# Performance work log

Hardware: AMD Instinct MI355X
Metric: run time of the kernel (lower is better)

Reference implementation:

```python
import jax, jax.numpy as jnp
import numpy as np

EMBED_DIMS = 1024
NUM_HEADS = 16
HEAD_DIMS = EMBED_DIMS // NUM_HEADS


def setup_inputs() -> dict:
    key = jax.random.key(0)
    k_x, k_wqkv, k_bqkv, k_wp, k_bp = jax.random.split(key, 5)
    B, N, D = 2, 2048, EMBED_DIMS
    x = jax.random.normal(k_x, (B, N, D), dtype=jnp.float32)
    # torch nn.Linear(in, out): weight [out, in], y = x @ W.T + b
    s = 1.0 / np.sqrt(D)
    W_qkv = jax.random.uniform(k_wqkv, (3 * D, D), jnp.float32, -s, s)
    b_qkv = jax.random.uniform(k_bqkv, (3 * D,), jnp.float32, -s, s)
    W_proj = jax.random.uniform(k_wp, (D, D), jnp.float32, -s, s)
    b_proj = jax.random.uniform(k_bp, (D,), jnp.float32, -s, s)
    return {"x": x, "W_qkv": W_qkv, "b_qkv": b_qkv, "W_proj": W_proj, "b_proj": b_proj}


def reference(x, W_qkv, b_qkv, W_proj, b_proj):
    B, N, D = x.shape
    H, Hd = NUM_HEADS, HEAD_DIMS
    # qkv projection: [B, N, 3, H, Hd] -> split q, k, v as [B, H, N, Hd]
    qkv = (x @ W_qkv.T + b_qkv).reshape(B, N, 3, H, Hd).transpose(2, 0, 3, 1, 4)
    q, k, v = qkv[0], qkv[1], qkv[2]
    scale = 1.0 / jnp.sqrt(jnp.asarray(Hd, x.dtype))
    attn = jnp.einsum("bhqd,bhkd->bhqk", q, k) * scale  # [B, H, N, N]
    attn = jax.nn.softmax(attn, axis=-1)
    out = jnp.einsum("bhqk,bhkd->bhqd", attn, v)  # [B, H, N, Hd]
    out = out.transpose(0, 2, 1, 3).reshape(B, N, D)
    out = out @ W_proj.T + b_proj
    return out
```

## Files before the change

### kernel.cpp

```cpp
#include <hip/hip_runtime.h>

typedef _Float16 f16x8 __attribute__((ext_vector_type(8)));
typedef __attribute__((ext_vector_type(4))) float f32x4;

static __device__ __forceinline__ unsigned short f2h(float f) {
  return __builtin_bit_cast(unsigned short, (_Float16)f);
}

#if __has_builtin(__builtin_amdgcn_exp2f)
#define EXP2(x) __builtin_amdgcn_exp2f(x)
#else
#define EXP2(x) exp2f(x)
#endif

#define GLOAD_LDS16(gp, lp)                                          \
  __builtin_amdgcn_global_load_lds(                                  \
      (const __attribute__((address_space(1))) unsigned int*)(gp),   \
      (__attribute__((address_space(3))) unsigned int*)(lp), 16, 0, 0)

__global__ __launch_bounds__(256) void cvt_all(
    const float* __restrict__ X, const float* __restrict__ Wq,
    const float* __restrict__ Wp, unsigned short* __restrict__ Xb,
    unsigned short* __restrict__ Wqb, unsigned short* __restrict__ Wpb) {
  const int i = blockIdx.x * 256 + threadIdx.x;
  const float4* src;
  unsigned short* dst;
  int off;
  if (i < 1048576) {
    src = (const float4*)X; dst = Xb; off = i;
  } else if (i < 1835008) {
    src = (const float4*)Wq; dst = Wqb; off = i - 1048576;
  } else {
    src = (const float4*)Wp; dst = Wpb; off = i - 1835008;
  }
  const float4 v = src[off];
  *(ushort4*)(dst + (size_t)off * 4) =
      make_ushort4(f2h(v.x), f2h(v.y), f2h(v.z), f2h(v.w));
}

__global__ __launch_bounds__(256) void qkv_gemm(
    const unsigned short* __restrict__ Xb, const unsigned short* __restrict__ Wb,
    const float* __restrict__ bias, unsigned short* __restrict__ Qb,
    unsigned short* __restrict__ Kb, unsigned short* __restrict__ Vt) {
  __shared__ __align__(16) unsigned short A_sh[128 * 32];
  __shared__ __align__(16) unsigned short B_sh[128 * 32];
  const int n0 = blockIdx.x * 128, m0 = blockIdx.y * 128;
  const int tid = threadIdx.x, lane = tid & 63, wave = tid >> 6;
  const int wr = wave >> 1, wc = wave & 1, lm = lane & 15, lg = lane >> 4;
  const int lrow = lane >> 2, lcol = (lane & 3) * 8;

  f32x4 acc[4][4] = {};

  for (int k0 = 0; k0 < 1024; k0 += 32) {
#pragma unroll
    for (int j = 0; j < 2; ++j) {
      const int chunk = wave * 2 + j;
      const int row = chunk * 16 + lrow;
      GLOAD_LDS16(Xb + (size_t)(m0 + row) * 1024 + k0 + lcol, &A_sh[chunk * 512]);
      GLOAD_LDS16(Wb + (size_t)(n0 + row) * 1024 + k0 + lcol, &B_sh[chunk * 512]);
    }
    __syncthreads();
    f16x8 af[4], bfr[4];
#pragma unroll
    for (int mi = 0; mi < 4; ++mi)
      af[mi] = *(const f16x8*)&A_sh[(wr * 64 + mi * 16 + lm) * 32 + lg * 8];
#pragma unroll
    for (int ni = 0; ni < 4; ++ni)
      bfr[ni] = *(const f16x8*)&B_sh[(wc * 64 + ni * 16 + lm) * 32 + lg * 8];
#pragma unroll
    for (int mi = 0; mi < 4; ++mi)
#pragma unroll
      for (int ni = 0; ni < 4; ++ni)
        acc[mi][ni] = __builtin_amdgcn_mfma_f32_16x16x32_f16(
            af[mi], bfr[ni], acc[mi][ni], 0, 0, 0);
    __syncthreads();
  }

  const float qscale = 0.18033688011112042f;
#pragma unroll
  for (int mi = 0; mi < 4; ++mi) {
#pragma unroll
    for (int ni = 0; ni < 4; ++ni) {
      const int gn = n0 + wc * 64 + ni * 16 + lm;
      const float bv = bias[gn];
      const int which = gn >> 10;
      const int h = (gn >> 6) & 15;
      const int hd = gn & 63;
      float v[4];
#pragma unroll
      for (int r = 0; r < 4; ++r) v[r] = acc[mi][ni][r] + bv;
      const int gm0 = m0 + wr * 64 + mi * 16 + lg * 4;
      const int bb = gm0 >> 11;
      const int nq0 = gm0 & 2047;
      if (which == 0) {
        unsigned short* p = Qb + (((size_t)bb * 16 + h) * 2048 + nq0) * 64 + hd;
        p[0] = f2h(v[0] * qscale);   p[64] = f2h(v[1] * qscale);
        p[128] = f2h(v[2] * qscale); p[192] = f2h(v[3] * qscale);
      } else if (which == 1) {
        unsigned short* p = Kb + (((size_t)bb * 16 + h) * 2048 + nq0) * 64 + hd;
        p[0] = f2h(v[0]);   p[64] = f2h(v[1]);
        p[128] = f2h(v[2]); p[192] = f2h(v[3]);
      } else {
        *(ushort4*)(Vt + (((size_t)bb * 16 + h) * 64 + hd) * 2048 + nq0) =
            make_ushort4(f2h(v[0]), f2h(v[1]), f2h(v[2]), f2h(v[3]));
      }
    }
  }
}

__global__ __launch_bounds__(256) void attn_kernel(
    const unsigned short* __restrict__ Qb, const unsigned short* __restrict__ Kb,
    const unsigned short* __restrict__ Vt, unsigned short* __restrict__ Ob) {
  __shared__ __align__(16) unsigned short K_sh[2][2][64 * 32];
  __shared__ __align__(16) unsigned short V_sh[2][2][64 * 32];
  __shared__ __align__(16) unsigned short P_sh[128 * 68];
  const int bh = blockIdx.y, q0 = blockIdx.x * 128;
  const size_t base = (size_t)bh * (2048 * 64);
  const unsigned short* Qp = Qb + base;
  const unsigned short* Kp = Kb + base;
  const unsigned short* Vp = Vt + base;
  const int tid = threadIdx.x, lane = tid & 63, wave = tid >> 6;
  const int lm = lane & 15, lg = lane >> 4;
  const int r4 = lane >> 2;
  const int sg8 = (((lane & 3) ^ ((r4 >> 1) & 3)) * 8);
  const int lgx = (lg ^ ((lm >> 1) & 3)) * 8;

  f16x8 qf[2][2];
#pragma unroll
  for (int mi = 0; mi < 2; ++mi)
#pragma unroll
    for (int kc = 0; kc < 2; ++kc)
      qf[mi][kc] = *(const f16x8*)(Qp +
          (size_t)(q0 + wave * 32 + mi * 16 + lm) * 64 + kc * 32 + lg * 8);

  f32x4 o[2][4] = {};
  float lsum[2][4] = {};

  const int plane = wave & 1;
  const bool isV = wave >= 2;

#define STAGE(kt_, b_)                                                        \
  do {                                                                        \
    if (!isV) {                                                               \
      _Pragma("unroll")                                                       \
      for (int qv = 0; qv < 4; ++qv)                                          \
        GLOAD_LDS16(Kp + (size_t)((kt_) * 64 + qv * 16 + r4) * 64 +           \
                        plane * 32 + sg8,                                     \
                    &K_sh[b_][plane][qv * 512]);                              \
    } else {                                                                  \
      _Pragma("unroll")                                                       \
      for (int qv = 0; qv < 4; ++qv)                                          \
        GLOAD_LDS16(Vp + (size_t)(qv * 16 + r4) * 2048 + (kt_) * 64 +         \
                        plane * 32 + sg8,                                     \
                    &V_sh[b_][plane][qv * 512]);                              \
    }                                                                         \
  } while (0)

  STAGE(0, 0);

  for (int kt = 0; kt < 32; ++kt) {
    const int cur = kt & 1;
    __syncthreads();
    if (kt < 31) STAGE(kt + 1, cur ^ 1);

    f32x4 s[2][4] = {};
#pragma unroll
    for (int kc = 0; kc < 2; ++kc) {
#pragma unroll
      for (int ni = 0; ni < 4; ++ni) {
        const f16x8 kf =
            *(const f16x8*)&K_sh[cur][kc][(ni * 16 + lm) * 32 + lgx];
#pragma unroll
        for (int mi = 0; mi < 2; ++mi)
          s[mi][ni] = __builtin_amdgcn_mfma_f32_16x16x32_f16(
              qf[mi][kc], kf, s[mi][ni], 0, 0, 0);
      }
    }

#pragma unroll
    for (int mi = 0; mi < 2; ++mi)
#pragma unroll
      for (int ni = 0; ni < 4; ++ni) {
        float p0 = EXP2(s[mi][ni][0]), p1 = EXP2(s[mi][ni][1]);
        float p2 = EXP2(s[mi][ni][2]), p3 = EXP2(s[mi][ni][3]);
        lsum[mi][0] += p0; lsum[mi][1] += p1;
        lsum[mi][2] += p2; lsum[mi][3] += p3;
        unsigned short* pp =
            &P_sh[(wave * 32 + mi * 16 + lg * 4) * 68 + ni * 16 + lm];
        pp[0] = f2h(p0);    pp[68] = f2h(p1);
        pp[136] = f2h(p2);  pp[204] = f2h(p3);
      }

#pragma unroll
    for (int kc = 0; kc < 2; ++kc) {
      f16x8 pa[2];
#pragma unroll
      for (int mi = 0; mi < 2; ++mi)
        pa[mi] = *(const f16x8*)&P_sh[(wave * 32 + mi * 16 + lm) * 68 +
                                      kc * 32 + lg * 8];
#pragma unroll
      for (int ni = 0; ni < 4; ++ni) {
        const f16x8 vb =
            *(const f16x8*)&V_sh[cur][kc][(ni * 16 + lm) * 32 + lgx];
#pragma unroll
        for (int mi = 0; mi < 2; ++mi)
          o[mi][ni] = __builtin_amdgcn_mfma_f32_16x16x32_f16(
              pa[mi], vb, o[mi][ni], 0, 0, 0);
      }
    }
  }
#undef STAGE

  const int b = bh >> 4, h = bh & 15;
#pragma unroll
  for (int mi = 0; mi < 2; ++mi)
#pragma unroll
    for (int r = 0; r < 4; ++r) {
      float l = lsum[mi][r];
      l += __shfl_xor(l, 1);
      l += __shfl_xor(l, 2);
      l += __shfl_xor(l, 4);
      l += __shfl_xor(l, 8);
      const float inv = 1.0f / l;
      const int nq = q0 + wave * 32 + mi * 16 + lg * 4 + r;
      unsigned short* p = Ob + ((size_t)(b * 2048 + nq) * 16 + h) * 64 + lm;
      p[0] = f2h(o[mi][0][r] * inv);
      p[16] = f2h(o[mi][1][r] * inv);
      p[32] = f2h(o[mi][2][r] * inv);
      p[48] = f2h(o[mi][3][r] * inv);
    }
}

__global__ __launch_bounds__(256) void proj_gemm(
    const unsigned short* __restrict__ A, const unsigned short* __restrict__ Wb,
    const float* __restrict__ bias, float* __restrict__ Out) {
  __shared__ __align__(16) unsigned short A_sh[64 * 32];
  __shared__ __align__(16) unsigned short B_sh[128 * 32];
  const int n0 = blockIdx.x * 128, m0 = blockIdx.y * 64;
  const int tid = threadIdx.x, lane = tid & 63, wave = tid >> 6;
  const int wr = wave >> 1, wc = wave & 1, lm = lane & 15, lg = lane >> 4;
  const int lrow = lane >> 2, lcol = (lane & 3) * 8;

  f32x4 acc[2][4] = {};

  for (int k0 = 0; k0 < 1024; k0 += 32) {
    {
      const int row = wave * 16 + lrow;
      GLOAD_LDS16(A + (size_t)(m0 + row) * 1024 + k0 + lcol, &A_sh[wave * 512]);
    }
#pragma unroll
    for (int j = 0; j < 2; ++j) {
      const int chunk = wave * 2 + j;
      const int row = chunk * 16 + lrow;
      GLOAD_LDS16(Wb + (size_t)(n0 + row) * 1024 + k0 + lcol, &B_sh[chunk * 512]);
    }
    __syncthreads();
    f16x8 af[2], bfr[4];
#pragma unroll
    for (int mi = 0; mi < 2; ++mi)
      af[mi] = *(const f16x8*)&A_sh[(wr * 32 + mi * 16 + lm) * 32 + lg * 8];
#pragma unroll
    for (int ni = 0; ni < 4; ++ni)
      bfr[ni] = *(const f16x8*)&B_sh[(wc * 64 + ni * 16 + lm) * 32 + lg * 8];
#pragma unroll
    for (int mi = 0; mi < 2; ++mi)
#pragma unroll
      for (int ni = 0; ni < 4; ++ni)
        acc[mi][ni] = __builtin_amdgcn_mfma_f32_16x16x32_f16(
            af[mi], bfr[ni], acc[mi][ni], 0, 0, 0);
    __syncthreads();
  }

#pragma unroll
  for (int mi = 0; mi < 2; ++mi)
#pragma unroll
    for (int ni = 0; ni < 4; ++ni) {
      const int gn = n0 + wc * 64 + ni * 16 + lm;
      const float bv = bias[gn];
#pragma unroll
      for (int r = 0; r < 4; ++r) {
        const int gm = m0 + wr * 32 + mi * 16 + lg * 4 + r;
        Out[(size_t)gm * 1024 + gn] = acc[mi][ni][r] + bv;
      }
    }
}

extern "C" void kernel_launch(void* const* d_in, const int* in_sizes, int n_in,
                              void* d_out, int out_size, void* d_ws, size_t ws_size,
                              hipStream_t stream) {
  const float* x      = (const float*)d_in[0];
  const float* W_qkv  = (const float*)d_in[1];
  const float* b_qkv  = (const float*)d_in[2];
  const float* W_proj = (const float*)d_in[3];
  const float* b_proj = (const float*)d_in[4];
  float* out = (float*)d_out;

  unsigned short* Qb  = (unsigned short*)d_ws;
  unsigned short* Kb  = Qb + 4194304;
  unsigned short* Vt  = Kb + 4194304;
  unsigned short* Ao  = Vt + 4194304;
  unsigned short* Xb  = Ao + 4194304;
  unsigned short* Wqb = Xb + 4194304;
  unsigned short* Wpb = Wqb + 3145728;

  cvt_all<<<8192, 256, 0, stream>>>(x, W_qkv, W_proj, Xb, Wqb, Wpb);
  qkv_gemm<<<dim3(24, 32), 256, 0, stream>>>(Xb, Wqb, b_qkv, Qb, Kb, Vt);
  attn_kernel<<<dim3(16, 32), 256, 0, stream>>>(Qb, Kb, Vt, Ao);
  proj_gemm<<<dim3(8, 64), 256, 0, stream>>>(Ao, Wpb, b_proj, out);
}
```

Before: 197.8 us.

## Widen GEMM K-step with swizzled LDS and halve attention query tile

The QKV and projection GEMMs now load a 64-wide K slab per iteration into two 32-wide LDS planes, using an XOR-swizzled layout. This halves the number of barrier pairs per K loop and aims to reduce LDS bank conflicts. The attention kernel drops from 128 to 64 query rows per block, with 16 rows per wave, which doubles the grid to improve occupancy and wave count across CUs. The cost is that each block now streams the full K/V sequence for fewer query rows, so K/V traffic per unit of work doubles, and the larger GEMM LDS footprint may lower occupancy.

```diff
diff --git a/kernel.cpp b/kernel.cpp
--- a/kernel.cpp
+++ b/kernel.cpp
@@ -42,37 +42,47 @@
     const unsigned short* __restrict__ Xb, const unsigned short* __restrict__ Wb,
     const float* __restrict__ bias, unsigned short* __restrict__ Qb,
     unsigned short* __restrict__ Kb, unsigned short* __restrict__ Vt) {
-  __shared__ __align__(16) unsigned short A_sh[128 * 32];
-  __shared__ __align__(16) unsigned short B_sh[128 * 32];
+  __shared__ __align__(16) unsigned short A_sh[2][128 * 32];
+  __shared__ __align__(16) unsigned short B_sh[2][128 * 32];
   const int n0 = blockIdx.x * 128, m0 = blockIdx.y * 128;
   const int tid = threadIdx.x, lane = tid & 63, wave = tid >> 6;
   const int wr = wave >> 1, wc = wave & 1, lm = lane & 15, lg = lane >> 4;
-  const int lrow = lane >> 2, lcol = (lane & 3) * 8;
+  const int r4 = lane >> 2;
+  const int sg8 = (((lane & 3) ^ ((r4 >> 1) & 3)) * 8);
+  const int lgx = (lg ^ ((lm >> 1) & 3)) * 8;
 
   f32x4 acc[4][4] = {};
 
-  for (int k0 = 0; k0 < 1024; k0 += 32) {
+  for (int k0 = 0; k0 < 1024; k0 += 64) {
 #pragma unroll
     for (int j = 0; j < 2; ++j) {
       const int chunk = wave * 2 + j;
-      const int row = chunk * 16 + lrow;
-      GLOAD_LDS16(Xb + (size_t)(m0 + row) * 1024 + k0 + lcol, &A_sh[chunk * 512]);
-      GLOAD_LDS16(Wb + (size_t)(n0 + row) * 1024 + k0 + lcol, &B_sh[chunk * 512]);
-    }
-    __syncthreads();
-    f16x8 af[4], bfr[4];
-#pragma unroll
-    for (int mi = 0; mi < 4; ++mi)
-      af[mi] = *(const f16x8*)&A_sh[(wr * 64 + mi * 16 + lm) * 32 + lg * 8];
-#pragma unroll
-    for (int ni = 0; ni < 4; ++ni)
-      bfr[ni] = *(const f16x8*)&B_sh[(wc * 64 + ni * 16 + lm) * 32 + lg * 8];
-#pragma unroll
-    for (int mi = 0; mi < 4; ++mi)
+      const int row = chunk * 16 + r4;
+#pragma unroll
+      for (int p = 0; p < 2; ++p) {
+        GLOAD_LDS16(Xb + (size_t)(m0 + row) * 1024 + k0 + p * 32 + sg8,
+                    &A_sh[p][chunk * 512]);
+        GLOAD_LDS16(Wb + (size_t)(n0 + row) * 1024 + k0 + p * 32 + sg8,
+                    &B_sh[p][chunk * 512]);
+      }
+    }
+    __syncthreads();
+#pragma unroll
+    for (int kc = 0; kc < 2; ++kc) {
+      f16x8 af[4], bfr[4];
+#pragma unroll
+      for (int mi = 0; mi < 4; ++mi)
+        af[mi] = *(const f16x8*)&A_sh[kc][(wr * 64 + mi * 16 + lm) * 32 + lgx];
 #pragma unroll
       for (int ni = 0; ni < 4; ++ni)
-        acc[mi][ni] = __builtin_amdgcn_mfma_f32_16x16x32_f16(
-            af[mi], bfr[ni], acc[mi][ni], 0, 0, 0);
+        bfr[ni] = *(const f16x8*)&B_sh[kc][(wc * 64 + ni * 16 + lm) * 32 + lgx];
+#pragma unroll
+      for (int mi = 0; mi < 4; ++mi)
+#pragma unroll
+        for (int ni = 0; ni < 4; ++ni)
+          acc[mi][ni] = __builtin_amdgcn_mfma_f32_16x16x32_f16(
+              af[mi], bfr[ni], acc[mi][ni], 0, 0, 0);
+    }
     __syncthreads();
   }
 
@@ -113,8 +123,8 @@
     const unsigned short* __restrict__ Vt, unsigned short* __restrict__ Ob) {
   __shared__ __align__(16) unsigned short K_sh[2][2][64 * 32];
   __shared__ __align__(16) unsigned short V_sh[2][2][64 * 32];
-  __shared__ __align__(16) unsigned short P_sh[128 * 68];
-  const int bh = blockIdx.y, q0 = blockIdx.x * 128;
+  __shared__ __align__(16) unsigned short P_sh[64 * 68];
+  const int bh = blockIdx.y, q0 = blockIdx.x * 64;
   const size_t base = (size_t)bh * (2048 * 64);
   const unsigned short* Qp = Qb + base;
   const unsigned short* Kp = Kb + base;
@@ -125,16 +135,14 @@
   const int sg8 = (((lane & 3) ^ ((r4 >> 1) & 3)) * 8);
   const int lgx = (lg ^ ((lm >> 1) & 3)) * 8;
 
-  f16x8 qf[2][2];
-#pragma unroll
-  for (int mi = 0; mi < 2; ++mi)
-#pragma unroll
-    for (int kc = 0; kc < 2; ++kc)
-      qf[mi][kc] = *(const f16x8*)(Qp +
-          (size_t)(q0 + wave * 32 + mi * 16 + lm) * 64 + kc * 32 + lg * 8);
-
-  f32x4 o[2][4] = {};
-  float lsum[2][4] = {};
+  f16x8 qf[2];
+#pragma unroll
+  for (int kc = 0; kc < 2; ++kc)
+    qf[kc] = *(const f16x8*)(Qp +
+        (size_t)(q0 + wave * 16 + lm) * 64 + kc * 32 + lg * 8);
+
+  f32x4 o[4] = {};
+  float lsum[4] = {};
 
   const int plane = wave & 1;
   const bool isV = wave >= 2;
@@ -163,49 +171,36 @@
     __syncthreads();
     if (kt < 31) STAGE(kt + 1, cur ^ 1);
 
-    f32x4 s[2][4] = {};
+    f32x4 s[4] = {};
 #pragma unroll
     for (int kc = 0; kc < 2; ++kc) {
 #pragma unroll
       for (int ni = 0; ni < 4; ++ni) {
         const f16x8 kf =
             *(const f16x8*)&K_sh[cur][kc][(ni * 16 + lm) * 32 + lgx];
-#pragma unroll
-        for (int mi = 0; mi < 2; ++mi)
-          s[mi][ni] = __builtin_amdgcn_mfma_f32_16x16x32_f16(
-              qf[mi][kc], kf, s[mi][ni], 0, 0, 0);
-      }
-    }
-
-#pragma unroll
-    for (int mi = 0; mi < 2; ++mi)
-#pragma unroll
-      for (int ni = 0; ni < 4; ++ni) {
-        float p0 = EXP2(s[mi][ni][0]), p1 = EXP2(s[mi][ni][1]);
-        float p2 = EXP2(s[mi][ni][2]), p3 = EXP2(s[mi][ni][3]);
-        lsum[mi][0] += p0; lsum[mi][1] += p1;
-        lsum[mi][2] += p2; lsum[mi][3] += p3;
-        unsigned short* pp =
-            &P_sh[(wave * 32 + mi * 16 + lg * 4) * 68 + ni * 16 + lm];
-        pp[0] = f2h(p0);    pp[68] = f2h(p1);
-        pp[136] = f2h(p2);  pp[204] = f2h(p3);
-      }
+        s[ni] = __builtin_amdgcn_mfma_f32_16x16x32_f16(qf[kc], kf, s[ni], 0, 0, 0);
+      }
+    }
+
+#pragma unroll
+    for (int ni = 0; ni < 4; ++ni) {
+      float p0 = EXP2(s[ni][0]), p1 = EXP2(s[ni][1]);
+      float p2 = EXP2(s[ni][2]), p3 = EXP2(s[ni][3]);
+      lsum[0] += p0; lsum[1] += p1; lsum[2] += p2; lsum[3] += p3;
+      unsigned short* pp = &P_sh[(wave * 16 + lg * 4) * 68 + ni * 16 + lm];
+      pp[0] = f2h(p0);    pp[68] = f2h(p1);
+      pp[136] = f2h(p2);  pp[204] = f2h(p3);
+    }
 
 #pragma unroll
     for (int kc = 0; kc < 2; ++kc) {
-      f16x8 pa[2];
-#pragma unroll
-      for (int mi = 0; mi < 2; ++mi)
-        pa[mi] = *(const f16x8*)&P_sh[(wave * 32 + mi * 16 + lm) * 68 +
-                                      kc * 32 + lg * 8];
+      const f16x8 pa =
+          *(const f16x8*)&P_sh[(wave * 16 + lm) * 68 + kc * 32 + lg * 8];
 #pragma unroll
       for (int ni = 0; ni < 4; ++ni) {
         const f16x8 vb =
             *(const f16x8*)&V_sh[cur][kc][(ni * 16 + lm) * 32 + lgx];
-#pragma unroll
-        for (int mi = 0; mi < 2; ++mi)
-          o[mi][ni] = __builtin_amdgcn_mfma_f32_16x16x32_f16(
-              pa[mi], vb, o[mi][ni], 0, 0, 0);
+        o[ni] = __builtin_amdgcn_mfma_f32_16x16x32_f16(pa, vb, o[ni], 0, 0, 0);
       }
     }
   }
@@ -213,61 +208,70 @@
 
   const int b = bh >> 4, h = bh & 15;
 #pragma unroll
-  for (int mi = 0; mi < 2; ++mi)
-#pragma unroll
-    for (int r = 0; r < 4; ++r) {
-      float l = lsum[mi][r];
-      l += __shfl_xor(l, 1);
-      l += __shfl_xor(l, 2);
-      l += __shfl_xor(l, 4);
-      l += __shfl_xor(l, 8);
-      const float inv = 1.0f / l;
-      const int nq = q0 + wave * 32 + mi * 16 + lg * 4 + r;
-      unsigned short* p = Ob + ((size_t)(b * 2048 + nq) * 16 + h) * 64 + lm;
-      p[0] = f2h(o[mi][0][r] * inv);
-      p[16] = f2h(o[mi][1][r] * inv);
-      p[32] = f2h(o[mi][2][r] * inv);
-      p[48] = f2h(o[mi][3][r] * inv);
-    }
+  for (int r = 0; r < 4; ++r) {
+    float l = lsum[r];
+    l += __shfl_xor(l, 1);
+    l += __shfl_xor(l, 2);
+    l += __shfl_xor(l, 4);
+    l += __shfl_xor(l, 8);
+    const float inv = 1.0f / l;
+    const int nq = q0 + wave * 16 + lg * 4 + r;
+    unsigned short* p = Ob + ((size_t)(b * 2048 + nq) * 16 + h) * 64 + lm;
+    p[0] = f2h(o[0][r] * inv);
+    p[16] = f2h(o[1][r] * inv);
+    p[32] = f2h(o[2][r] * inv);
+    p[48] = f2h(o[3][r] * inv);
+  }
 }
 
 __global__ __launch_bounds__(256) void proj_gemm(
     const unsigned short* __restrict__ A, const unsigned short* __restrict__ Wb,
     const float* __restrict__ bias, float* __restrict__ Out) {
-  __shared__ __align__(16) unsigned short A_sh[64 * 32];
-  __shared__ __align__(16) unsigned short B_sh[128 * 32];
+  __shared__ __align__(16) unsigned short A_sh[2][64 * 32];
+  __shared__ __align__(16) unsigned short B_sh[2][128 * 32];
   const int n0 = blockIdx.x * 128, m0 = blockIdx.y * 64;
   const int tid = threadIdx.x, lane = tid & 63, wave = tid >> 6;
   const int wr = wave >> 1, wc = wave & 1, lm = lane & 15, lg = lane >> 4;
-  const int lrow = lane >> 2, lcol = (lane & 3) * 8;
+  const int r4 = lane >> 2;
+  const int sg8 = (((lane & 3) ^ ((r4 >> 1) & 3)) * 8);
+  const int lgx = (lg ^ ((lm >> 1) & 3)) * 8;
 
   f32x4 acc[2][4] = {};
 
-  for (int k0 = 0; k0 < 1024; k0 += 32) {
+  for (int k0 = 0; k0 < 1024; k0 += 64) {
     {
-      const int row = wave * 16 + lrow;
-      GLOAD_LDS16(A + (size_t)(m0 + row) * 1024 + k0 + lcol, &A_sh[wave * 512]);
+      const int row = wave * 16 + r4;
+#pragma unroll
+      for (int p = 0; p < 2; ++p)
+        GLOAD_LDS16(A + (size_t)(m0 + row) * 1024 + k0 + p * 32 + sg8,
+                    &A_sh[p][wave * 512]);
     }
 #pragma unroll
     for (int j = 0; j < 2; ++j) {
       const int chunk = wave * 2 + j;
-      const int row = chunk * 16 + lrow;
-      GLOAD_LDS16(Wb + (size_t)(n0 + row) * 1024 + k0 + lcol, &B_sh[chunk * 512]);
-    }
-    __syncthreads();
-    f16x8 af[2], bfr[4];
-#pragma unroll
-    for (int mi = 0; mi < 2; ++mi)
-      af[mi] = *(const f16x8*)&A_sh[(wr * 32 + mi * 16 + lm) * 32 + lg * 8];
-#pragma unroll
-    for (int ni = 0; ni < 4; ++ni)
-      bfr[ni] = *(const f16x8*)&B_sh[(wc * 64 + ni * 16 + lm) * 32 + lg * 8];
-#pragma unroll
-    for (int mi = 0; mi < 2; ++mi)
+      const int row = chunk * 16 + r4;
+#pragma unroll
+      for (int p = 0; p < 2; ++p)
+        GLOAD_LDS16(Wb + (size_t)(n0 + row) * 1024 + k0 + p * 32 + sg8,
+                    &B_sh[p][chunk * 512]);
+    }
+    __syncthreads();
+#pragma unroll
+    for (int kc = 0; kc < 2; ++kc) {
+      f16x8 af[2], bfr[4];
+#pragma unroll
+      for (int mi = 0; mi < 2; ++mi)
+        af[mi] = *(const f16x8*)&A_sh[kc][(wr * 32 + mi * 16 + lm) * 32 + lgx];
 #pragma unroll
       for (int ni = 0; ni < 4; ++ni)
-        acc[mi][ni] = __builtin_amdgcn_mfma_f32_16x16x32_f16(
-            af[mi], bfr[ni], acc[mi][ni], 0, 0, 0);
+        bfr[ni] = *(const f16x8*)&B_sh[kc][(wc * 64 + ni * 16 + lm) * 32 + lgx];
+#pragma unroll
+      for (int mi = 0; mi < 2; ++mi)
+#pragma unroll
+        for (int ni = 0; ni < 4; ++ni)
+          acc[mi][ni] = __builtin_amdgcn_mfma_f32_16x16x32_f16(
+              af[mi], bfr[ni], acc[mi][ni], 0, 0, 0);
+    }
     __syncthreads();
   }
 
@@ -305,6 +309,6 @@
 
   cvt_all<<<8192, 256, 0, stream>>>(x, W_qkv, W_proj, Xb, Wqb, Wpb);
   qkv_gemm<<<dim3(24, 32), 256, 0, stream>>>(Xb, Wqb, b_qkv, Qb, Kb, Vt);
-  attn_kernel<<<dim3(16, 32), 256, 0, stream>>>(Qb, Kb, Vt, Ao);
+  attn_kernel<<<dim3(32, 32), 256, 0, stream>>>(Qb, Kb, Vt, Ao);
   proj_gemm<<<dim3(8, 64), 256, 0, stream>>>(Ao, Wpb, b_proj, out);
 }
```

Measured after the change: 213.6 us. 8.0% more time.
